# Optimization experiments

Hardware: AMD Instinct MI355X
Metric: run time of the kernel (lower is better)

The kernel has to match this reference:

```python
import jax, jax.numpy as jnp
import numpy as np

ALPHA = 1.702   # GLU sigmoid scale
LIMIT = 7.0     # clamp limit
K = 2           # experts per token


def setup_inputs() -> dict:
    key = jax.random.key(0)
    ks = jax.random.split(key, 4)
    B, S, H, E, I = 1, 1024, 1024, 8, 1024
    return {
        "hidden_states": jax.random.normal(ks[0], (B, S, H), jnp.float32),
        "router_weight": jax.random.normal(ks[1], (E, H), jnp.float32),
        "router_bias": jnp.zeros((E,), jnp.float32),
        "gate_up_proj": jax.random.normal(ks[2], (E, H, 2 * I), jnp.float32) * 0.02,
        "gate_up_bias": jnp.zeros((E, 2 * I), jnp.float32),
        "down_proj": jax.random.normal(ks[3], (E, I, H), jnp.float32) * 0.02,
        "down_bias": jnp.zeros((E, H), jnp.float32),
    }


def reference(hidden_states, router_weight, router_bias, gate_up_proj,
              gate_up_bias, down_proj, down_bias):
    B, S, H = hidden_states.shape
    E = router_weight.shape[0]
    I = down_proj.shape[1]
    T = B * S

    flat = hidden_states.reshape(T, H)

    # Router: softmax over experts, top-K selection (weights NOT renormalized).
    logits = flat @ router_weight.T + router_bias               # [T, E]
    scores = jax.nn.softmax(logits, axis=-1)
    topk_vals, topk_idx = jax.lax.top_k(scores, K)              # [T, K]

    # Dense per-token expert weight matrix (equivalent of dispatch metadata +
    # combine * topk_weights in the tt pipeline); top-k indices are unique.
    w = jnp.zeros((T, E), scores.dtype).at[
        jnp.arange(T)[:, None], topk_idx].set(topk_vals)        # [T, E]

    # Expert MLP with clamped GLU (gpt-oss style).
    gu = jnp.einsum('th,ehf->tef', flat, gate_up_proj) + gate_up_bias  # [T,E,2I]
    gate = jnp.minimum(gu[..., :I], LIMIT)
    up = jnp.clip(gu[..., I:], -LIMIT, LIMIT)
    glu = gate * jax.nn.sigmoid(gate * ALPHA)
    act = (up + 1.0) * glu                                       # [T, E, I]

    down = jnp.einsum('tei,eih->teh', act, down_proj) + down_bias  # [T, E, H]

    # Weighted combine over selected experts.
    out = jnp.einsum('teh,te->th', down, w)
    return out.reshape(B, S, H)
```

## Files before the change

kernel.cpp:

```cpp
#include <hip/hip_runtime.h>
#include <hip/hip_bf16.h>


typedef unsigned short u16;
typedef __attribute__((ext_vector_type(8))) __bf16 bf16x8;
typedef __attribute__((ext_vector_type(4))) float f32x4;

#define T_TOK 1024
#define H_DIM 1024
#define E_NUM 8
#define I_DIM 1024
#define ALPHA 1.702f
#define LIMIT 7.0f
#define LSTR 72

__device__ __forceinline__ u16 f2bf(float f) {
    unsigned u = __builtin_bit_cast(unsigned, f);
    u = (u + 0x7FFFu + ((u >> 16) & 1u)) >> 16;
    return (u16)u;
}

__device__ __forceinline__ unsigned pk2(float lo, float hi) {
#if defined(__has_builtin) && __has_builtin(__builtin_amdgcn_cvt_pk_bf16_f32)
    typedef __attribute__((ext_vector_type(2))) __bf16 bf16x2_t;
    bf16x2_t v = __builtin_amdgcn_cvt_pk_bf16_f32(lo, hi);
    return __builtin_bit_cast(unsigned, v);
#else
    return (unsigned)f2bf(lo) | ((unsigned)f2bf(hi) << 16);
#endif
}

__device__ __forceinline__ f32x4 mfma16(bf16x8 a, bf16x8 b, f32x4 c) {
    return __builtin_amdgcn_mfma_f32_16x16x32_bf16(a, b, c, 0, 0, 0);
}

__device__ __forceinline__ void expert_range(const int* counts, int e,
                                             int& cnt, int& abase) {
    int a = 0, c = 0;
#pragma unroll
    for (int i = 0; i < E_NUM; ++i) {
        int v = counts[i];
        if (i < e) a += v;
        if (i == e) c = v;
    }
    cnt = c; abase = a;
}

__global__ void k_zero(int* counts) {
    if (threadIdx.x < E_NUM) counts[threadIdx.x] = 0;
}

__global__ __launch_bounds__(256) void k_router(
    const float* __restrict__ x, const float* __restrict__ rw,
    const float* __restrict__ rb, const float* __restrict__ db,
    int* __restrict__ counts, int* __restrict__ tok_list,
    float* __restrict__ w_list, u16* __restrict__ xb,
    float* __restrict__ out)
{
    const int t = blockIdx.x;
    const int tid = threadIdx.x;
    const float4 xv = *(const float4*)(x + (size_t)t * H_DIM + tid * 4);

    *(uint2*)(xb + (size_t)t * H_DIM + tid * 4) =
        make_uint2(pk2(xv.x, xv.y), pk2(xv.z, xv.w));

    float p[E_NUM];
#pragma unroll
    for (int e = 0; e < E_NUM; ++e) {
        const float4 wv = *(const float4*)(rw + e * H_DIM + tid * 4);
        p[e] = xv.x * wv.x + xv.y * wv.y + xv.z * wv.z + xv.w * wv.w;
    }
#pragma unroll
    for (int off = 32; off; off >>= 1) {
#pragma unroll
        for (int e = 0; e < E_NUM; ++e) p[e] += __shfl_down(p[e], off, 64);
    }
    __shared__ float red[4][E_NUM];
    __shared__ int se[2];
    __shared__ float sw[2];
    const int lane = tid & 63, wvid = tid >> 6;
    if (lane == 0) {
#pragma unroll
        for (int e = 0; e < E_NUM; ++e) red[wvid][e] = p[e];
    }
    __syncthreads();
    if (tid == 0) {
        float lg[E_NUM];
#pragma unroll
        for (int e = 0; e < E_NUM; ++e)
            lg[e] = red[0][e] + red[1][e] + red[2][e] + red[3][e] + rb[e];
        float m1 = -1e30f, m2 = -1e30f; int i1 = 0, i2 = 0;
#pragma unroll
        for (int e = 0; e < E_NUM; ++e) {
            float l = lg[e];
            if (l > m1) { m2 = m1; i2 = i1; m1 = l; i1 = e; }
            else if (l > m2) { m2 = l; i2 = e; }
        }
        float s = 0.f;
#pragma unroll
        for (int e = 0; e < E_NUM; ++e) s += __expf(lg[e] - m1);
        const float w0 = 1.0f / s;
        const float w1 = __expf(m2 - m1) / s;
        int slot0 = atomicAdd(&counts[i1], 1);
        tok_list[i1 * T_TOK + slot0] = t;
        w_list[i1 * T_TOK + slot0] = w0;
        int slot1 = atomicAdd(&counts[i2], 1);
        tok_list[i2 * T_TOK + slot1] = t;
        w_list[i2 * T_TOK + slot1] = w1;
        se[0] = i1; se[1] = i2; sw[0] = w0; sw[1] = w1;
    }
    __syncthreads();
    const int e0 = se[0], e1 = se[1];
    const float w0 = sw[0], w1 = sw[1];
    const int c = tid * 4;
    float4 d0 = *(const float4*)(db + e0 * H_DIM + c);
    float4 d1 = *(const float4*)(db + e1 * H_DIM + c);
    float4 o;
    o.x = w0 * d0.x + w1 * d1.x;
    o.y = w0 * d0.y + w1 * d1.y;
    o.z = w0 * d0.z + w1 * d1.z;
    o.w = w0 * d0.w + w1 * d1.w;
    *(float4*)(out + (size_t)t * H_DIM + c) = o;
}

__global__ __launch_bounds__(256) void k_gateup(
    const float* __restrict__ gup, const float* __restrict__ gub,
    const int* __restrict__ counts, const int* __restrict__ tok_list,
    const u16* __restrict__ xb, u16* __restrict__ act)
{
    const int e = blockIdx.z;
    int cnt, abase;
    expert_range(counts, e, cnt, abase);
    const int m0 = blockIdx.y * 64;
    if (m0 >= cnt) return;
    const int n0 = blockIdx.x * 32;
    const int tid = threadIdx.x;

    __shared__ __align__(16) u16 As[64 * LSTR];
    __shared__ __align__(16) u16 Bs[64 * LSTR];
    unsigned* Bs32 = (unsigned*)Bs;

    const int arow_i = tid >> 2, akq = (tid & 3) * 16;
    const int aslot = m0 + arow_i;
    const int atok = (aslot < cnt) ? tok_list[e * T_TOK + aslot] : 0;
    const u16* asrc = xb + (size_t)atok * H_DIM + akq;
    u16* adst = &As[arow_i * LSTR + akq];

    const int kp = tid >> 3, q = tid & 7;
    const float* bgate = gup + ((size_t)e << 21) + n0 + q * 4;

    const int lane = tid & 63, wv = tid >> 6;
    const int fm = lane & 15, kg = lane >> 4;

    f32x4 accg[2], accu[2];
#pragma unroll
    for (int nt = 0; nt < 2; ++nt) {
        accg[nt] = (f32x4){0.f, 0.f, 0.f, 0.f};
        accu[nt] = (f32x4){0.f, 0.f, 0.f, 0.f};
    }

#define GU_LOAD(A0, A1, G0, G1, U0, U1, KB)                                    \
    {                                                                          \
        const u16* ap_ = asrc + (KB);                                          \
        A0 = *(const uint4*)(ap_);                                             \
        A1 = *(const uint4*)(ap_ + 8);                                         \
        const float* gp_ = bgate + (size_t)((KB) + 2 * kp) * 2048;             \
        G0 = *(const float4*)(gp_);                                            \
        G1 = *(const float4*)(gp_ + 2048);                                     \
        U0 = *(const float4*)(gp_ + 1024);                                     \
        U1 = *(const float4*)(gp_ + 3072);                                     \
    }
#define GU_STORE(A0, A1, G0, G1, U0, U1)                                       \
    {                                                                          \
        *(uint4*)adst       = A0;                                              \
        *(uint4*)(adst + 8) = A1;                                              \
        const float* g0_ = (const float*)&G0; const float* g1_ = (const float*)&G1; \
        const float* u0_ = (const float*)&U0; const float* u1_ = (const float*)&U1; \
        _Pragma("unroll")                                                      \
        for (int j = 0; j < 4; ++j) {                                          \
            Bs32[(q * 4 + j) * 36 + kp]        = pk2(g0_[j], g1_[j]);          \
            Bs32[(32 + q * 4 + j) * 36 + kp]   = pk2(u0_[j], u1_[j]);          \
        }                                                                      \
    }
#define GU_MFMA()                                                              \
    {                                                                          \
        _Pragma("unroll")                                                      \
        for (int sub = 0; sub < 2; ++sub) {                                    \
            bf16x8 af = *(const bf16x8*)&As[(wv * 16 + fm) * LSTR + sub * 32 + kg * 8]; \
            _Pragma("unroll")                                                  \
            for (int nt = 0; nt < 2; ++nt) {                                   \
                bf16x8 bg = *(const bf16x8*)&Bs[(nt * 16 + fm) * LSTR + sub * 32 + kg * 8]; \
                bf16x8 bu = *(const bf16x8*)&Bs[(32 + nt * 16 + fm) * LSTR + sub * 32 + kg * 8]; \
                accg[nt] = mfma16(af, bg, accg[nt]);                           \
                accu[nt] = mfma16(af, bu, accu[nt]);                           \
            }                                                                  \
        }                                                                      \
    }

    uint4 a0s0, a1s0, a0s1, a1s1;
    float4 g0s0, g1s0, u0s0, u1s0, g0s1, g1s1, u0s1, u1s1;
    GU_LOAD(a0s0, a1s0, g0s0, g1s0, u0s0, u1s0, 0);
    GU_LOAD(a0s1, a1s1, g0s1, g1s1, u0s1, u1s1, 64);

    for (int kb = 0; kb < H_DIM; kb += 128) {
        __syncthreads();
        GU_STORE(a0s0, a1s0, g0s0, g1s0, u0s0, u1s0);
        if (kb + 128 < H_DIM) GU_LOAD(a0s0, a1s0, g0s0, g1s0, u0s0, u1s0, kb + 128);
        __syncthreads();
        GU_MFMA();

        __syncthreads();
        GU_STORE(a0s1, a1s1, g0s1, g1s1, u0s1, u1s1);
        if (kb + 192 < H_DIM) GU_LOAD(a0s1, a1s1, g0s1, g1s1, u0s1, u1s1, kb + 192);
        __syncthreads();
        GU_MFMA();
    }
#undef GU_LOAD
#undef GU_STORE
#undef GU_MFMA

#pragma unroll
    for (int r = 0; r < 4; ++r) {
        int rowb = wv * 16 + kg * 4 + r;
        int slot = m0 + rowb;
        if (slot >= cnt) continue;
        size_t arow_o = (size_t)(abase + slot) * I_DIM;
#pragma unroll
        for (int nt = 0; nt < 2; ++nt) {
            int cn = n0 + nt * 16 + fm;
            float g = accg[nt][r] + gub[e * 2048 + cn];
            float u = accu[nt][r] + gub[e * 2048 + 1024 + cn];
            g = fminf(g, LIMIT);
            u = fminf(fmaxf(u, -LIMIT), LIMIT);
            float glu = g / (1.f + __expf(-ALPHA * g));
            act[arow_o + cn] = f2bf((u + 1.f) * glu);
        }
    }
}

__global__ __launch_bounds__(256) void k_down(
    const float* __restrict__ dp,
    const int* __restrict__ counts, const int* __restrict__ tok_list,
    const float* __restrict__ w_list,
    const u16* __restrict__ act, float* __restrict__ out)
{
    const int e = blockIdx.z & 7, ks = blockIdx.z >> 3;
    int cnt, abase;
    expert_range(counts, e, cnt, abase);
    const int m0 = blockIdx.y * 64;
    if (m0 >= cnt) return;
    const int n0 = blockIdx.x * 64;
    const int tid = threadIdx.x;

    __shared__ __align__(16) u16 As[64 * LSTR];
    __shared__ __align__(16) u16 Bs[64 * LSTR];
    unsigned* Bs32 = (unsigned*)Bs;

    const int arow_i = tid >> 2, akq = (tid & 3) * 16;
    const u16* asrc = act + (size_t)(abase + m0 + arow_i) * I_DIM + ks * 512 + akq;
    u16* adst = &As[arow_i * LSTR + akq];

    const int kp = tid >> 3, q = tid & 7;
    const float* bsrc = dp + ((size_t)e << 20) + (size_t)(ks * 512) * 1024 + n0 + q * 4;

    const int lane = tid & 63, wv = tid >> 6;
    const int fm = lane & 15, kg = lane >> 4;

    f32x4 acc[4];
#pragma unroll
    for (int nt = 0; nt < 4; ++nt) acc[nt] = (f32x4){0.f, 0.f, 0.f, 0.f};

#define DN_LOAD(A0, A1, B00, B01, B10, B11, KB)                                \
    {                                                                          \
        const u16* ap_ = asrc + (KB);                                          \
        A0 = *(const uint4*)(ap_);                                             \
        A1 = *(const uint4*)(ap_ + 8);                                         \
        const float* bp_ = bsrc + (size_t)((KB) + 2 * kp) * 1024;              \
        B00 = *(const float4*)(bp_);                                           \
        B01 = *(const float4*)(bp_ + 1024);                                    \
        B10 = *(const float4*)(bp_ + 32);                                      \
        B11 = *(const float4*)(bp_ + 1056);                                    \
    }
#define DN_STORE(A0, A1, B00, B01, B10, B11)                                   \
    {                                                                          \
        *(uint4*)adst       = A0;                                              \
        *(uint4*)(adst + 8) = A1;                                              \
        const float* b00_ = (const float*)&B00; const float* b01_ = (const float*)&B01; \
        const float* b10_ = (const float*)&B10; const float* b11_ = (const float*)&B11; \
        _Pragma("unroll")                                                      \
        for (int j = 0; j < 4; ++j) {                                          \
            Bs32[(q * 4 + j) * 36 + kp]      = pk2(b00_[j], b01_[j]);          \
            Bs32[(32 + q * 4 + j) * 36 + kp] = pk2(b10_[j], b11_[j]);          \
        }                                                                      \
    }
#define DN_MFMA()                                                              \
    {                                                                          \
        _Pragma("unroll")                                                      \
        for (int sub = 0; sub < 2; ++sub) {                                    \
            bf16x8 af = *(const bf16x8*)&As[(wv * 16 + fm) * LSTR + sub * 32 + kg * 8]; \
            _Pragma("unroll")                                                  \
            for (int nt = 0; nt < 4; ++nt) {                                   \
                bf16x8 b = *(const bf16x8*)&Bs[(nt * 16 + fm) * LSTR + sub * 32 + kg * 8]; \
                acc[nt] = mfma16(af, b, acc[nt]);                              \
            }                                                                  \
        }                                                                      \
    }

    uint4 a0s0, a1s0, a0s1, a1s1;
    float4 b00s0, b01s0, b10s0, b11s0, b00s1, b01s1, b10s1, b11s1;
    DN_LOAD(a0s0, a1s0, b00s0, b01s0, b10s0, b11s0, 0);
    DN_LOAD(a0s1, a1s1, b00s1, b01s1, b10s1, b11s1, 64);

    for (int kb = 0; kb < 512; kb += 128) {
        __syncthreads();
        DN_STORE(a0s0, a1s0, b00s0, b01s0, b10s0, b11s0);
        if (kb + 128 < 512) DN_LOAD(a0s0, a1s0, b00s0, b01s0, b10s0, b11s0, kb + 128);
        __syncthreads();
        DN_MFMA();

        __syncthreads();
        DN_STORE(a0s1, a1s1, b00s1, b01s1, b10s1, b11s1);
        if (kb + 192 < 512) DN_LOAD(a0s1, a1s1, b00s1, b01s1, b10s1, b11s1, kb + 192);
        __syncthreads();
        DN_MFMA();
    }
#undef DN_LOAD
#undef DN_STORE
#undef DN_MFMA

#pragma unroll
    for (int r = 0; r < 4; ++r) {
        int rowb = wv * 16 + kg * 4 + r;
        int slot = m0 + rowb;
        if (slot >= cnt) continue;
        float wgt = w_list[e * T_TOK + slot];
        int tok = tok_list[e * T_TOK + slot];
        float* orow = out + (size_t)tok * H_DIM + n0;
#pragma unroll
        for (int nt = 0; nt < 4; ++nt)
            atomicAdd(orow + nt * 16 + fm, acc[nt][r] * wgt);
    }
}

extern "C" void kernel_launch(void* const* d_in, const int* in_sizes, int n_in,
                              void* d_out, int out_size, void* d_ws, size_t ws_size,
                              hipStream_t stream) {
    const float* x   = (const float*)d_in[0];
    const float* rw  = (const float*)d_in[1];
    const float* rb  = (const float*)d_in[2];
    const float* gup = (const float*)d_in[3];
    const float* gub = (const float*)d_in[4];
    const float* dp  = (const float*)d_in[5];
    const float* db  = (const float*)d_in[6];
    float* out = (float*)d_out;

    char* ws = (char*)d_ws;
    int*   counts   = (int*)(ws);
    int*   tok_list = (int*)(ws + 64);
    float* w_list   = (float*)(ws + 64 + 32768);
    u16*   xb       = (u16*)(ws + 65600);
    u16*   act      = (u16*)(ws + 65600 + 2097152);

    k_zero<<<1, 64, 0, stream>>>(counts);
    k_router<<<T_TOK, 256, 0, stream>>>(x, rw, rb, db, counts, tok_list, w_list,
                                        xb, out);
    k_gateup<<<dim3(32, 16, 8), 256, 0, stream>>>(gup, gub, counts, tok_list,
                                                  xb, act);
    k_down<<<dim3(16, 16, 16), 256, 0, stream>>>(dp, counts, tok_list, w_list,
                                                 act, out);
}
```

Baseline: 212.0 us.

## Double-buffer LDS tiles and replace atomic combine with separate reduction kernel

The gate-up and down GEMM main loops now use two LDS buffers, so each step needs only one barrier instead of two and the next tile's store overlaps the current MFMA work. The down kernel writes weighted partial results per K-split into a scratch buffer instead of doing float atomicAdd into the output. A new combine kernel sums the two expert contributions and the two K-split partials per token and adds the bias. The zeroing kernel is replaced by a memset. This adds an extra launch and extra scratch-buffer traffic in exchange for removing atomic contention and halving barriers.

```diff
diff --git a/kernel.cpp b/kernel.cpp
--- a/kernel.cpp
+++ b/kernel.cpp
@@ -13,6 +13,8 @@
 #define ALPHA 1.702f
 #define LIMIT 7.0f
 #define LSTR 72
+#define AROWS 2112
+#define DPART (AROWS * 1024)
 
 __device__ __forceinline__ u16 f2bf(float f) {
     unsigned u = __builtin_bit_cast(unsigned, f);
@@ -46,16 +48,12 @@
     cnt = c; abase = a;
 }
 
-__global__ void k_zero(int* counts) {
-    if (threadIdx.x < E_NUM) counts[threadIdx.x] = 0;
-}
-
 __global__ __launch_bounds__(256) void k_router(
     const float* __restrict__ x, const float* __restrict__ rw,
-    const float* __restrict__ rb, const float* __restrict__ db,
-    int* __restrict__ counts, int* __restrict__ tok_list,
-    float* __restrict__ w_list, u16* __restrict__ xb,
-    float* __restrict__ out)
+    const float* __restrict__ rb,
+    int* __restrict__ counts, int* __restrict__ tk_e, int* __restrict__ tk_slot,
+    float* __restrict__ tk_w, int* __restrict__ tok_list,
+    float* __restrict__ w_list, u16* __restrict__ xb)
 {
     const int t = blockIdx.x;
     const int tid = threadIdx.x;
@@ -76,8 +74,6 @@
         for (int e = 0; e < E_NUM; ++e) p[e] += __shfl_down(p[e], off, 64);
     }
     __shared__ float red[4][E_NUM];
-    __shared__ int se[2];
-    __shared__ float sw[2];
     const int lane = tid & 63, wvid = tid >> 6;
     if (lane == 0) {
 #pragma unroll
@@ -101,26 +97,19 @@
         for (int e = 0; e < E_NUM; ++e) s += __expf(lg[e] - m1);
         const float w0 = 1.0f / s;
         const float w1 = __expf(m2 - m1) / s;
-        int slot0 = atomicAdd(&counts[i1], 1);
-        tok_list[i1 * T_TOK + slot0] = t;
-        w_list[i1 * T_TOK + slot0] = w0;
-        int slot1 = atomicAdd(&counts[i2], 1);
-        tok_list[i2 * T_TOK + slot1] = t;
-        w_list[i2 * T_TOK + slot1] = w1;
-        se[0] = i1; se[1] = i2; sw[0] = w0; sw[1] = w1;
-    }
-    __syncthreads();
-    const int e0 = se[0], e1 = se[1];
-    const float w0 = sw[0], w1 = sw[1];
-    const int c = tid * 4;
-    float4 d0 = *(const float4*)(db + e0 * H_DIM + c);
-    float4 d1 = *(const float4*)(db + e1 * H_DIM + c);
-    float4 o;
-    o.x = w0 * d0.x + w1 * d1.x;
-    o.y = w0 * d0.y + w1 * d1.y;
-    o.z = w0 * d0.z + w1 * d1.z;
-    o.w = w0 * d0.w + w1 * d1.w;
-    *(float4*)(out + (size_t)t * H_DIM + c) = o;
+        int ee[2] = { i1, i2 };
+        float ww[2] = { w0, w1 };
+#pragma unroll
+        for (int k = 0; k < 2; ++k) {
+            int e = ee[k];
+            int slot = atomicAdd(&counts[e], 1);
+            tok_list[e * T_TOK + slot] = t;
+            w_list[e * T_TOK + slot] = ww[k];
+            tk_e[t * 2 + k] = e;
+            tk_slot[t * 2 + k] = slot;
+            tk_w[t * 2 + k] = ww[k];
+        }
+    }
 }
 
 __global__ __launch_bounds__(256) void k_gateup(
@@ -136,15 +125,14 @@
     const int n0 = blockIdx.x * 32;
     const int tid = threadIdx.x;
 
-    __shared__ __align__(16) u16 As[64 * LSTR];
-    __shared__ __align__(16) u16 Bs[64 * LSTR];
-    unsigned* Bs32 = (unsigned*)Bs;
-
+    __shared__ __align__(16) u16 As[2][64 * LSTR];
+    __shared__ __align__(16) u16 Bs[2][64 * LSTR];
+    
     const int arow_i = tid >> 2, akq = (tid & 3) * 16;
     const int aslot = m0 + arow_i;
     const int atok = (aslot < cnt) ? tok_list[e * T_TOK + aslot] : 0;
     const u16* asrc = xb + (size_t)atok * H_DIM + akq;
-    u16* adst = &As[arow_i * LSTR + akq];
+    const int aoff = arow_i * LSTR + akq;
 
     const int kp = tid >> 3, q = tid & 7;
     const float* bgate = gup + ((size_t)e << 21) + n0 + q * 4;
@@ -159,61 +147,65 @@
         accu[nt] = (f32x4){0.f, 0.f, 0.f, 0.f};
     }
 
-#define GU_LOAD(A0, A1, G0, G1, U0, U1, KB)                                    \
-    {                                                                          \
-        const u16* ap_ = asrc + (KB);                                          \
+#define GU_LOAD(A0, A1, G0, G1, U0, U1, CH)                                    \
+    {                                                                          \
+        const u16* ap_ = asrc + (CH) * 64;                                     \
         A0 = *(const uint4*)(ap_);                                             \
         A1 = *(const uint4*)(ap_ + 8);                                         \
-        const float* gp_ = bgate + (size_t)((KB) + 2 * kp) * 2048;             \
+        const float* gp_ = bgate + (size_t)((CH) * 64 + 2 * kp) * 2048;        \
         G0 = *(const float4*)(gp_);                                            \
         G1 = *(const float4*)(gp_ + 2048);                                     \
         U0 = *(const float4*)(gp_ + 1024);                                     \
         U1 = *(const float4*)(gp_ + 3072);                                     \
     }
-#define GU_STORE(A0, A1, G0, G1, U0, U1)                                       \
-    {                                                                          \
-        *(uint4*)adst       = A0;                                              \
-        *(uint4*)(adst + 8) = A1;                                              \
+#define GU_STORE(BUF, A0, A1, G0, G1, U0, U1)                                  \
+    {                                                                          \
+        *(uint4*)&As[BUF][aoff]     = A0;                                      \
+        *(uint4*)&As[BUF][aoff + 8] = A1;                                      \
+        unsigned* b32_ = (unsigned*)&Bs[BUF][0];                               \
         const float* g0_ = (const float*)&G0; const float* g1_ = (const float*)&G1; \
         const float* u0_ = (const float*)&U0; const float* u1_ = (const float*)&U1; \
         _Pragma("unroll")                                                      \
         for (int j = 0; j < 4; ++j) {                                          \
-            Bs32[(q * 4 + j) * 36 + kp]        = pk2(g0_[j], g1_[j]);          \
-            Bs32[(32 + q * 4 + j) * 36 + kp]   = pk2(u0_[j], u1_[j]);          \
+            b32_[(q * 4 + j) * 36 + kp]      = pk2(g0_[j], g1_[j]);            \
+            b32_[(32 + q * 4 + j) * 36 + kp] = pk2(u0_[j], u1_[j]);            \
         }                                                                      \
     }
-#define GU_MFMA()                                                              \
+#define GU_MFMA(BUF)                                                           \
     {                                                                          \
         _Pragma("unroll")                                                      \
         for (int sub = 0; sub < 2; ++sub) {                                    \
-            bf16x8 af = *(const bf16x8*)&As[(wv * 16 + fm) * LSTR + sub * 32 + kg * 8]; \
+            bf16x8 af = *(const bf16x8*)&As[BUF][(wv * 16 + fm) * LSTR + sub * 32 + kg * 8]; \
             _Pragma("unroll")                                                  \
             for (int nt = 0; nt < 2; ++nt) {                                   \
-                bf16x8 bg = *(const bf16x8*)&Bs[(nt * 16 + fm) * LSTR + sub * 32 + kg * 8]; \
-                bf16x8 bu = *(const bf16x8*)&Bs[(32 + nt * 16 + fm) * LSTR + sub * 32 + kg * 8]; \
+                bf16x8 bg = *(const bf16x8*)&Bs[BUF][(nt * 16 + fm) * LSTR + sub * 32 + kg * 8]; \
+                bf16x8 bu = *(const bf16x8*)&Bs[BUF][(32 + nt * 16 + fm) * LSTR + sub * 32 + kg * 8]; \
                 accg[nt] = mfma16(af, bg, accg[nt]);                           \
                 accu[nt] = mfma16(af, bu, accu[nt]);                           \
             }                                                                  \
         }                                                                      \
     }
 
-    uint4 a0s0, a1s0, a0s1, a1s1;
-    float4 g0s0, g1s0, u0s0, u1s0, g0s1, g1s1, u0s1, u1s1;
-    GU_LOAD(a0s0, a1s0, g0s0, g1s0, u0s0, u1s0, 0);
-    GU_LOAD(a0s1, a1s1, g0s1, g1s1, u0s1, u1s1, 64);
-
-    for (int kb = 0; kb < H_DIM; kb += 128) {
+    uint4 a0r0, a1r0, a0r1, a1r1;
+    float4 g0r0, g1r0, u0r0, u1r0, g0r1, g1r1, u0r1, u1r1;
+    GU_LOAD(a0r0, a1r0, g0r0, g1r0, u0r0, u1r0, 0);
+    GU_LOAD(a0r1, a1r1, g0r1, g1r1, u0r1, u1r1, 1);
+    GU_STORE(0, a0r0, a1r0, g0r0, g1r0, u0r0, u1r0);
+    GU_LOAD(a0r0, a1r0, g0r0, g1r0, u0r0, u1r0, 2);
+
+#pragma unroll 4
+    for (int i = 0; i < 16; ++i) {
         __syncthreads();
-        GU_STORE(a0s0, a1s0, g0s0, g1s0, u0s0, u1s0);
-        if (kb + 128 < H_DIM) GU_LOAD(a0s0, a1s0, g0s0, g1s0, u0s0, u1s0, kb + 128);
-        __syncthreads();
-        GU_MFMA();
-
-        __syncthreads();
-        GU_STORE(a0s1, a1s1, g0s1, g1s1, u0s1, u1s1);
-        if (kb + 192 < H_DIM) GU_LOAD(a0s1, a1s1, g0s1, g1s1, u0s1, u1s1, kb + 192);
-        __syncthreads();
-        GU_MFMA();
+        const int b = i & 1;
+        if (i < 15) {
+            if (b == 0) { GU_STORE(1, a0r1, a1r1, g0r1, g1r1, u0r1, u1r1); }
+            else        { GU_STORE(0, a0r0, a1r0, g0r0, g1r0, u0r0, u1r0); }
+        }
+        if (i < 13) {
+            if (b == 0) { GU_LOAD(a0r1, a1r1, g0r1, g1r1, u0r1, u1r1, i + 3); }
+            else        { GU_LOAD(a0r0, a1r0, g0r0, g1r0, u0r0, u1r0, i + 3); }
+        }
+        GU_MFMA(b);
     }
 #undef GU_LOAD
 #undef GU_STORE
@@ -240,9 +232,8 @@
 
 __global__ __launch_bounds__(256) void k_down(
     const float* __restrict__ dp,
-    const int* __restrict__ counts, const int* __restrict__ tok_list,
-    const float* __restrict__ w_list,
-    const u16* __restrict__ act, float* __restrict__ out)
+    const int* __restrict__ counts, const float* __restrict__ w_list,
+    const u16* __restrict__ act, float* __restrict__ dout)
 {
     const int e = blockIdx.z & 7, ks = blockIdx.z >> 3;
     int cnt, abase;
@@ -252,13 +243,12 @@
     const int n0 = blockIdx.x * 64;
     const int tid = threadIdx.x;
 
-    __shared__ __align__(16) u16 As[64 * LSTR];
-    __shared__ __align__(16) u16 Bs[64 * LSTR];
-    unsigned* Bs32 = (unsigned*)Bs;
+    __shared__ __align__(16) u16 As[2][64 * LSTR];
+    __shared__ __align__(16) u16 Bs[2][64 * LSTR];
 
     const int arow_i = tid >> 2, akq = (tid & 3) * 16;
     const u16* asrc = act + (size_t)(abase + m0 + arow_i) * I_DIM + ks * 512 + akq;
-    u16* adst = &As[arow_i * LSTR + akq];
+    const int aoff = arow_i * LSTR + akq;
 
     const int kp = tid >> 3, q = tid & 7;
     const float* bsrc = dp + ((size_t)e << 20) + (size_t)(ks * 512) * 1024 + n0 + q * 4;
@@ -270,59 +260,63 @@
 #pragma unroll
     for (int nt = 0; nt < 4; ++nt) acc[nt] = (f32x4){0.f, 0.f, 0.f, 0.f};
 
-#define DN_LOAD(A0, A1, B00, B01, B10, B11, KB)                                \
-    {                                                                          \
-        const u16* ap_ = asrc + (KB);                                          \
+#define DN_LOAD(A0, A1, B00, B01, B10, B11, CH)                                \
+    {                                                                          \
+        const u16* ap_ = asrc + (CH) * 64;                                     \
         A0 = *(const uint4*)(ap_);                                             \
         A1 = *(const uint4*)(ap_ + 8);                                         \
-        const float* bp_ = bsrc + (size_t)((KB) + 2 * kp) * 1024;              \
+        const float* bp_ = bsrc + (size_t)((CH) * 64 + 2 * kp) * 1024;         \
         B00 = *(const float4*)(bp_);                                           \
         B01 = *(const float4*)(bp_ + 1024);                                    \
         B10 = *(const float4*)(bp_ + 32);                                      \
         B11 = *(const float4*)(bp_ + 1056);                                    \
     }
-#define DN_STORE(A0, A1, B00, B01, B10, B11)                                   \
-    {                                                                          \
-        *(uint4*)adst       = A0;                                              \
-        *(uint4*)(adst + 8) = A1;                                              \
+#define DN_STORE(BUF, A0, A1, B00, B01, B10, B11)                              \
+    {                                                                          \
+        *(uint4*)&As[BUF][aoff]     = A0;                                      \
+        *(uint4*)&As[BUF][aoff + 8] = A1;                                      \
+        unsigned* b32_ = (unsigned*)&Bs[BUF][0];                               \
         const float* b00_ = (const float*)&B00; const float* b01_ = (const float*)&B01; \
         const float* b10_ = (const float*)&B10; const float* b11_ = (const float*)&B11; \
         _Pragma("unroll")                                                      \
         for (int j = 0; j < 4; ++j) {                                          \
-            Bs32[(q * 4 + j) * 36 + kp]      = pk2(b00_[j], b01_[j]);          \
-            Bs32[(32 + q * 4 + j) * 36 + kp] = pk2(b10_[j], b11_[j]);          \
+            b32_[(q * 4 + j) * 36 + kp]      = pk2(b00_[j], b01_[j]);          \
+            b32_[(32 + q * 4 + j) * 36 + kp] = pk2(b10_[j], b11_[j]);          \
         }                                                                      \
     }
-#define DN_MFMA()                                                              \
+#define DN_MFMA(BUF)                                                           \
     {                                                                          \
         _Pragma("unroll")                                                      \
         for (int sub = 0; sub < 2; ++sub) {                                    \
-            bf16x8 af = *(const bf16x8*)&As[(wv * 16 + fm) * LSTR + sub * 32 + kg * 8]; \
+            bf16x8 af = *(const bf16x8*)&As[BUF][(wv * 16 + fm) * LSTR + sub * 32 + kg * 8]; \
             _Pragma("unroll")                                                  \
             for (int nt = 0; nt < 4; ++nt) {                                   \
-                bf16x8 b = *(const bf16x8*)&Bs[(nt * 16 + fm) * LSTR + sub * 32 + kg * 8]; \
-                acc[nt] = mfma16(af, b, acc[nt]);                              \
+                bf16x8 bb = *(const bf16x8*)&Bs[BUF][(nt * 16 + fm) * LSTR + sub * 32 + kg * 8]; \
+                acc[nt] = mfma16(af, bb, acc[nt]);                             \
             }                                                                  \
         }                                                                      \
     }
 
-    uint4 a0s0, a1s0, a0s1, a1s1;
-    float4 b00s0, b01s0, b10s0, b11s0, b00s1, b01s1, b10s1, b11s1;
-    DN_LOAD(a0s0, a1s0, b00s0, b01s0, b10s0, b11s0, 0);
-    DN_LOAD(a0s1, a1s1, b00s1, b01s1, b10s1, b11s1, 64);
-
-    for (int kb = 0; kb < 512; kb += 128) {
+    uint4 a0r0, a1r0, a0r1, a1r1;
+    float4 b00r0, b01r0, b10r0, b11r0, b00r1, b01r1, b10r1, b11r1;
+    DN_LOAD(a0r0, a1r0, b00r0, b01r0, b10r0, b11r0, 0);
+    DN_LOAD(a0r1, a1r1, b00r1, b01r1, b10r1, b11r1, 1);
+    DN_STORE(0, a0r0, a1r0, b00r0, b01r0, b10r0, b11r0);
+    DN_LOAD(a0r0, a1r0, b00r0, b01r0, b10r0, b11r0, 2);
+
+#pragma unroll 4
+    for (int i = 0; i < 8; ++i) {
         __syncthreads();
-        DN_STORE(a0s0, a1s0, b00s0, b01s0, b10s0, b11s0);
-        if (kb + 128 < 512) DN_LOAD(a0s0, a1s0, b00s0, b01s0, b10s0, b11s0, kb + 128);
-        __syncthreads();
-        DN_MFMA();
-
-        __syncthreads();
-        DN_STORE(a0s1, a1s1, b00s1, b01s1, b10s1, b11s1);
-        if (kb + 192 < 512) DN_LOAD(a0s1, a1s1, b00s1, b01s1, b10s1, b11s1, kb + 192);
-        __syncthreads();
-        DN_MFMA();
+        const int b = i & 1;
+        if (i < 7) {
+            if (b == 0) { DN_STORE(1, a0r1, a1r1, b00r1, b01r1, b10r1, b11r1); }
+            else        { DN_STORE(0, a0r0, a1r0, b00r0, b01r0, b10r0, b11r0); }
+        }
+        if (i < 5) {
+            if (b == 0) { DN_LOAD(a0r1, a1r1, b00r1, b01r1, b10r1, b11r1, i + 3); }
+            else        { DN_LOAD(a0r0, a1r0, b00r0, b01r0, b10r0, b11r0, i + 3); }
+        }
+        DN_MFMA(b);
     }
 #undef DN_LOAD
 #undef DN_STORE
@@ -334,12 +328,40 @@
         int slot = m0 + rowb;
         if (slot >= cnt) continue;
         float wgt = w_list[e * T_TOK + slot];
-        int tok = tok_list[e * T_TOK + slot];
-        float* orow = out + (size_t)tok * H_DIM + n0;
+        size_t drow = (size_t)ks * DPART + (size_t)(abase + slot) * H_DIM;
 #pragma unroll
         for (int nt = 0; nt < 4; ++nt)
-            atomicAdd(orow + nt * 16 + fm, acc[nt][r] * wgt);
-    }
+            dout[drow + n0 + nt * 16 + fm] = acc[nt][r] * wgt;
+    }
+}
+
+__global__ __launch_bounds__(256) void k_combine(
+    const float* __restrict__ dout, const float* __restrict__ db,
+    const int* __restrict__ counts,
+    const int* __restrict__ tk_e, const int* __restrict__ tk_slot,
+    const float* __restrict__ tk_w, float* __restrict__ out)
+{
+    const int t = blockIdx.x, tid = threadIdx.x;
+    const int e0 = tk_e[t * 2], e1 = tk_e[t * 2 + 1];
+    int c0, a0base, c1, a1base;
+    expert_range(counts, e0, c0, a0base);
+    expert_range(counts, e1, c1, a1base);
+    const size_t p0 = (size_t)(a0base + tk_slot[t * 2]) * H_DIM;
+    const size_t p1 = (size_t)(a1base + tk_slot[t * 2 + 1]) * H_DIM;
+    const float w0 = tk_w[t * 2], w1 = tk_w[t * 2 + 1];
+    const int c = tid * 4;
+    float4 x0 = *(const float4*)(dout + p0 + c);
+    float4 x1 = *(const float4*)(dout + DPART + p0 + c);
+    float4 y0 = *(const float4*)(dout + p1 + c);
+    float4 y1 = *(const float4*)(dout + DPART + p1 + c);
+    float4 d0 = *(const float4*)(db + e0 * H_DIM + c);
+    float4 d1 = *(const float4*)(db + e1 * H_DIM + c);
+    float4 o;
+    o.x = x0.x + x1.x + y0.x + y1.x + w0 * d0.x + w1 * d1.x;
+    o.y = x0.y + x1.y + y0.y + y1.y + w0 * d0.y + w1 * d1.y;
+    o.z = x0.z + x1.z + y0.z + y1.z + w0 * d0.z + w1 * d1.z;
+    o.w = x0.w + x1.w + y0.w + y1.w + w0 * d0.w + w1 * d1.w;
+    *(float4*)(out + (size_t)t * H_DIM + c) = o;
 }
 
 extern "C" void kernel_launch(void* const* d_in, const int* in_sizes, int n_in,
@@ -356,16 +378,21 @@
 
     char* ws = (char*)d_ws;
     int*   counts   = (int*)(ws);
-    int*   tok_list = (int*)(ws + 64);
-    float* w_list   = (float*)(ws + 64 + 32768);
-    u16*   xb       = (u16*)(ws + 65600);
-    u16*   act      = (u16*)(ws + 65600 + 2097152);
-
-    k_zero<<<1, 64, 0, stream>>>(counts);
-    k_router<<<T_TOK, 256, 0, stream>>>(x, rw, rb, db, counts, tok_list, w_list,
-                                        xb, out);
+    int*   tk_e     = (int*)(ws + 64);
+    int*   tk_slot  = (int*)(ws + 8256);
+    float* tk_w     = (float*)(ws + 16448);
+    int*   tok_list = (int*)(ws + 24640);
+    float* w_list   = (float*)(ws + 57408);
+    u16*   xb       = (u16*)(ws + 90176);
+    u16*   act      = (u16*)(ws + 90176 + 2097152);
+    float* dout     = (float*)(ws + 90176 + 2097152 + 4325376);
+
+    hipMemsetAsync(counts, 0, 64, stream);
+    k_router<<<T_TOK, 256, 0, stream>>>(x, rw, rb, counts, tk_e, tk_slot, tk_w,
+                                        tok_list, w_list, xb);
     k_gateup<<<dim3(32, 16, 8), 256, 0, stream>>>(gup, gub, counts, tok_list,
                                                   xb, act);
-    k_down<<<dim3(16, 16, 16), 256, 0, stream>>>(dp, counts, tok_list, w_list,
-                                                 act, out);
-}
+    k_down<<<dim3(16, 16, 16), 256, 0, stream>>>(dp, counts, w_list, act, dout);
+    k_combine<<<T_TOK, 256, 0, stream>>>(dout, db, counts, tk_e, tk_slot, tk_w,
+                                         out);
+}
```

Measured after the change: 214.5 us. About the same (+1.2%).

## Pre-transpose weights to bf16 and enlarge GEMM tiles with double-buffered LDS

Applied to the files above, without the earlier changes.

Adds a prep kernel that converts the gate_up and down weights to bf16 and transposes them into a K-contiguous layout on every call. The GEMM kernels can then load B tiles with plain 16-byte vector loads, with no per-element packing when writing to shared memory. The M tile grows from 64 to 128 rows so each B tile is reused across more tokens. Shared memory becomes double-buffered with one barrier per step, and k_zero is replaced by hipMemsetAsync. The cost is an extra pass that reads the full fp32 weights and writes about 50 MB of bf16, plus larger register and LDS use per block.

```diff
diff --git a/kernel.cpp b/kernel.cpp
--- a/kernel.cpp
+++ b/kernel.cpp
@@ -13,6 +13,7 @@
 #define ALPHA 1.702f
 #define LIMIT 7.0f
 #define LSTR 72
+#define AROWS 2176
 
 __device__ __forceinline__ u16 f2bf(float f) {
     unsigned u = __builtin_bit_cast(unsigned, f);
@@ -44,10 +45,6 @@
         if (i == e) c = v;
     }
     cnt = c; abase = a;
-}
-
-__global__ void k_zero(int* counts) {
-    if (threadIdx.x < E_NUM) counts[threadIdx.x] = 0;
 }
 
 __global__ __launch_bounds__(256) void k_router(
@@ -123,123 +120,184 @@
     *(float4*)(out + (size_t)t * H_DIM + c) = o;
 }
 
+__global__ __launch_bounds__(256) void k_prep(
+    const float* __restrict__ gup, const float* __restrict__ dp,
+    u16* __restrict__ gup_t, u16* __restrict__ dp_t)
+{
+    __shared__ unsigned Lt[64 * 36];
+    const int bid = blockIdx.x;
+    const float* src; u16* dst; int C, ct, kt;
+    if (bid < 4096) {
+        int e = bid >> 9, t = bid & 511;
+        ct = t & 31; kt = t >> 5; C = 2048;
+        src = gup + ((size_t)e << 21);
+        dst = gup_t + ((size_t)e << 21);
+    } else {
+        int b2 = bid - 4096;
+        int e = b2 >> 8, t = b2 & 255;
+        ct = t & 15; kt = t >> 4; C = 1024;
+        src = dp + ((size_t)e << 20);
+        dst = dp_t + ((size_t)e << 20);
+    }
+    const int k0 = kt * 64, c0 = ct * 64;
+    const int tid = threadIdx.x;
+
+    const int kp = tid >> 3, q = tid & 7;
+    const float* s0 = src + (size_t)(k0 + 2 * kp) * C + c0 + q * 8;
+    float4 r0a = *(const float4*)(s0);
+    float4 r0b = *(const float4*)(s0 + 4);
+    float4 r1a = *(const float4*)(s0 + C);
+    float4 r1b = *(const float4*)(s0 + C + 4);
+    const float* e0 = (const float*)&r0a;
+    const float* e1 = (const float*)&r0b;
+    const float* f0 = (const float*)&r1a;
+    const float* f1 = (const float*)&r1b;
+#pragma unroll
+    for (int j = 0; j < 8; ++j) {
+        float lo = (j < 4) ? e0[j] : e1[j - 4];
+        float hi = (j < 4) ? f0[j] : f1[j - 4];
+        int cl = q * 8 + j;
+        int grp = (kp >> 2) ^ q;
+        Lt[cl * 36 + (grp << 2) + (kp & 3)] = pk2(lo, hi);
+    }
+    __syncthreads();
+
+    const int cl = tid >> 2, ko2 = tid & 3;
+#pragma unroll
+    for (int i = 0; i < 2; ++i) {
+        int koct = ko2 * 2 + i;
+        int grp = koct ^ (cl >> 3);
+        uint4 v = *(const uint4*)&Lt[cl * 36 + (grp << 2)];
+        *(uint4*)(dst + (size_t)(c0 + cl) * 1024 + k0 + koct * 8) = v;
+    }
+}
+
 __global__ __launch_bounds__(256) void k_gateup(
-    const float* __restrict__ gup, const float* __restrict__ gub,
+    const u16* __restrict__ gup_t, const float* __restrict__ gub,
     const int* __restrict__ counts, const int* __restrict__ tok_list,
     const u16* __restrict__ xb, u16* __restrict__ act)
 {
     const int e = blockIdx.z;
     int cnt, abase;
     expert_range(counts, e, cnt, abase);
-    const int m0 = blockIdx.y * 64;
+    const int m0 = blockIdx.y * 128;
     if (m0 >= cnt) return;
     const int n0 = blockIdx.x * 32;
     const int tid = threadIdx.x;
 
-    __shared__ __align__(16) u16 As[64 * LSTR];
-    __shared__ __align__(16) u16 Bs[64 * LSTR];
-    unsigned* Bs32 = (unsigned*)Bs;
-
-    const int arow_i = tid >> 2, akq = (tid & 3) * 16;
+    __shared__ __align__(16) u16 As[2][128 * LSTR];
+    __shared__ __align__(16) u16 Bs[2][64 * LSTR];
+
+    const int arow_i = tid >> 1, akh = (tid & 1) * 32;
     const int aslot = m0 + arow_i;
     const int atok = (aslot < cnt) ? tok_list[e * T_TOK + aslot] : 0;
-    const u16* asrc = xb + (size_t)atok * H_DIM + akq;
-    u16* adst = &As[arow_i * LSTR + akq];
-
-    const int kp = tid >> 3, q = tid & 7;
-    const float* bgate = gup + ((size_t)e << 21) + n0 + q * 4;
+    const u16* asrc = xb + (size_t)atok * H_DIM + akh;
+    const int aoff = arow_i * LSTR + akh;
+
+    const int cl = tid >> 3, koct = tid & 7;
+    const u16* bgs = gup_t + ((size_t)(e * 2048 + n0 + cl)) * 1024 + koct * 8;
+    const u16* bus = bgs + (size_t)1024 * 1024;
+    const int boffg = cl * LSTR + koct * 8;
+    const int boffu = (32 + cl) * LSTR + koct * 8;
 
     const int lane = tid & 63, wv = tid >> 6;
     const int fm = lane & 15, kg = lane >> 4;
 
-    f32x4 accg[2], accu[2];
-#pragma unroll
-    for (int nt = 0; nt < 2; ++nt) {
-        accg[nt] = (f32x4){0.f, 0.f, 0.f, 0.f};
-        accu[nt] = (f32x4){0.f, 0.f, 0.f, 0.f};
-    }
-
-#define GU_LOAD(A0, A1, G0, G1, U0, U1, KB)                                    \
-    {                                                                          \
-        const u16* ap_ = asrc + (KB);                                          \
+    f32x4 accg[2][2], accu[2][2];
+#pragma unroll
+    for (int mt = 0; mt < 2; ++mt)
+#pragma unroll
+        for (int nt = 0; nt < 2; ++nt) {
+            accg[mt][nt] = (f32x4){0.f, 0.f, 0.f, 0.f};
+            accu[mt][nt] = (f32x4){0.f, 0.f, 0.f, 0.f};
+        }
+
+#define GU_LOAD(A0, A1, A2, A3, G, U, CH)                                      \
+    {                                                                          \
+        const u16* ap_ = asrc + (CH) * 64;                                     \
         A0 = *(const uint4*)(ap_);                                             \
         A1 = *(const uint4*)(ap_ + 8);                                         \
-        const float* gp_ = bgate + (size_t)((KB) + 2 * kp) * 2048;             \
-        G0 = *(const float4*)(gp_);                                            \
-        G1 = *(const float4*)(gp_ + 2048);                                     \
-        U0 = *(const float4*)(gp_ + 1024);                                     \
-        U1 = *(const float4*)(gp_ + 3072);                                     \
-    }
-#define GU_STORE(A0, A1, G0, G1, U0, U1)                                       \
-    {                                                                          \
-        *(uint4*)adst       = A0;                                              \
-        *(uint4*)(adst + 8) = A1;                                              \
-        const float* g0_ = (const float*)&G0; const float* g1_ = (const float*)&G1; \
-        const float* u0_ = (const float*)&U0; const float* u1_ = (const float*)&U1; \
-        _Pragma("unroll")                                                      \
-        for (int j = 0; j < 4; ++j) {                                          \
-            Bs32[(q * 4 + j) * 36 + kp]        = pk2(g0_[j], g1_[j]);          \
-            Bs32[(32 + q * 4 + j) * 36 + kp]   = pk2(u0_[j], u1_[j]);          \
-        }                                                                      \
-    }
-#define GU_MFMA()                                                              \
+        A2 = *(const uint4*)(ap_ + 16);                                        \
+        A3 = *(const uint4*)(ap_ + 24);                                        \
+        G = *(const uint4*)(bgs + (CH) * 64);                                  \
+        U = *(const uint4*)(bus + (CH) * 64);                                  \
+    }
+#define GU_STORE(BUF, A0, A1, A2, A3, G, U)                                    \
+    {                                                                          \
+        *(uint4*)&As[BUF][aoff]      = A0;                                     \
+        *(uint4*)&As[BUF][aoff + 8]  = A1;                                     \
+        *(uint4*)&As[BUF][aoff + 16] = A2;                                     \
+        *(uint4*)&As[BUF][aoff + 24] = A3;                                     \
+        *(uint4*)&Bs[BUF][boffg] = G;                                          \
+        *(uint4*)&Bs[BUF][boffu] = U;                                          \
+    }
+#define GU_MFMA(BUF)                                                           \
     {                                                                          \
         _Pragma("unroll")                                                      \
         for (int sub = 0; sub < 2; ++sub) {                                    \
-            bf16x8 af = *(const bf16x8*)&As[(wv * 16 + fm) * LSTR + sub * 32 + kg * 8]; \
             _Pragma("unroll")                                                  \
-            for (int nt = 0; nt < 2; ++nt) {                                   \
-                bf16x8 bg = *(const bf16x8*)&Bs[(nt * 16 + fm) * LSTR + sub * 32 + kg * 8]; \
-                bf16x8 bu = *(const bf16x8*)&Bs[(32 + nt * 16 + fm) * LSTR + sub * 32 + kg * 8]; \
-                accg[nt] = mfma16(af, bg, accg[nt]);                           \
-                accu[nt] = mfma16(af, bu, accu[nt]);                           \
+            for (int mt = 0; mt < 2; ++mt) {                                   \
+                bf16x8 af = *(const bf16x8*)&As[BUF][(wv * 32 + mt * 16 + fm) * LSTR + sub * 32 + kg * 8]; \
+                _Pragma("unroll")                                              \
+                for (int nt = 0; nt < 2; ++nt) {                               \
+                    bf16x8 bg = *(const bf16x8*)&Bs[BUF][(nt * 16 + fm) * LSTR + sub * 32 + kg * 8]; \
+                    bf16x8 bu = *(const bf16x8*)&Bs[BUF][(32 + nt * 16 + fm) * LSTR + sub * 32 + kg * 8]; \
+                    accg[mt][nt] = mfma16(af, bg, accg[mt][nt]);               \
+                    accu[mt][nt] = mfma16(af, bu, accu[mt][nt]);               \
+                }                                                              \
             }                                                                  \
         }                                                                      \
     }
 
-    uint4 a0s0, a1s0, a0s1, a1s1;
-    float4 g0s0, g1s0, u0s0, u1s0, g0s1, g1s1, u0s1, u1s1;
-    GU_LOAD(a0s0, a1s0, g0s0, g1s0, u0s0, u1s0, 0);
-    GU_LOAD(a0s1, a1s1, g0s1, g1s1, u0s1, u1s1, 64);
-
-    for (int kb = 0; kb < H_DIM; kb += 128) {
+    uint4 A0r0, A1r0, A2r0, A3r0, Gr0, Ur0;
+    uint4 A0r1, A1r1, A2r1, A3r1, Gr1, Ur1;
+    GU_LOAD(A0r0, A1r0, A2r0, A3r0, Gr0, Ur0, 0);
+    GU_LOAD(A0r1, A1r1, A2r1, A3r1, Gr1, Ur1, 1);
+    GU_STORE(0, A0r0, A1r0, A2r0, A3r0, Gr0, Ur0);
+    GU_LOAD(A0r0, A1r0, A2r0, A3r0, Gr0, Ur0, 2);
+
+#pragma unroll 4
+    for (int i = 0; i < 16; ++i) {
         __syncthreads();
-        GU_STORE(a0s0, a1s0, g0s0, g1s0, u0s0, u1s0);
-        if (kb + 128 < H_DIM) GU_LOAD(a0s0, a1s0, g0s0, g1s0, u0s0, u1s0, kb + 128);
-        __syncthreads();
-        GU_MFMA();
-
-        __syncthreads();
-        GU_STORE(a0s1, a1s1, g0s1, g1s1, u0s1, u1s1);
-        if (kb + 192 < H_DIM) GU_LOAD(a0s1, a1s1, g0s1, g1s1, u0s1, u1s1, kb + 192);
-        __syncthreads();
-        GU_MFMA();
+        const int b = i & 1;
+        if (i < 15) {
+            if (b == 0) { GU_STORE(1, A0r1, A1r1, A2r1, A3r1, Gr1, Ur1); }
+            else        { GU_STORE(0, A0r0, A1r0, A2r0, A3r0, Gr0, Ur0); }
+        }
+        if (i < 13) {
+            if (b == 0) { GU_LOAD(A0r1, A1r1, A2r1, A3r1, Gr1, Ur1, i + 3); }
+            else        { GU_LOAD(A0r0, A1r0, A2r0, A3r0, Gr0, Ur0, i + 3); }
+        }
+        GU_MFMA(b);
     }
 #undef GU_LOAD
 #undef GU_STORE
 #undef GU_MFMA
 
 #pragma unroll
-    for (int r = 0; r < 4; ++r) {
-        int rowb = wv * 16 + kg * 4 + r;
-        int slot = m0 + rowb;
-        if (slot >= cnt) continue;
-        size_t arow_o = (size_t)(abase + slot) * I_DIM;
-#pragma unroll
-        for (int nt = 0; nt < 2; ++nt) {
-            int cn = n0 + nt * 16 + fm;
-            float g = accg[nt][r] + gub[e * 2048 + cn];
-            float u = accu[nt][r] + gub[e * 2048 + 1024 + cn];
-            g = fminf(g, LIMIT);
-            u = fminf(fmaxf(u, -LIMIT), LIMIT);
-            float glu = g / (1.f + __expf(-ALPHA * g));
-            act[arow_o + cn] = f2bf((u + 1.f) * glu);
+    for (int mt = 0; mt < 2; ++mt) {
+#pragma unroll
+        for (int r = 0; r < 4; ++r) {
+            int rowb = wv * 32 + mt * 16 + kg * 4 + r;
+            int slot = m0 + rowb;
+            if (slot >= cnt) continue;
+            size_t arow_o = (size_t)(abase + slot) * I_DIM;
+#pragma unroll
+            for (int nt = 0; nt < 2; ++nt) {
+                int cn = n0 + nt * 16 + fm;
+                float g = accg[mt][nt][r] + gub[e * 2048 + cn];
+                float u = accu[mt][nt][r] + gub[e * 2048 + 1024 + cn];
+                g = fminf(g, LIMIT);
+                u = fminf(fmaxf(u, -LIMIT), LIMIT);
+                float glu = g / (1.f + __expf(-ALPHA * g));
+                act[arow_o + cn] = f2bf((u + 1.f) * glu);
+            }
         }
     }
 }
 
 __global__ __launch_bounds__(256) void k_down(
-    const float* __restrict__ dp,
+    const u16* __restrict__ dp_t,
     const int* __restrict__ counts, const int* __restrict__ tok_list,
     const float* __restrict__ w_list,
     const u16* __restrict__ act, float* __restrict__ out)
@@ -247,98 +305,107 @@
     const int e = blockIdx.z & 7, ks = blockIdx.z >> 3;
     int cnt, abase;
     expert_range(counts, e, cnt, abase);
-    const int m0 = blockIdx.y * 64;
+    const int m0 = blockIdx.y * 128;
     if (m0 >= cnt) return;
     const int n0 = blockIdx.x * 64;
     const int tid = threadIdx.x;
 
-    __shared__ __align__(16) u16 As[64 * LSTR];
-    __shared__ __align__(16) u16 Bs[64 * LSTR];
-    unsigned* Bs32 = (unsigned*)Bs;
-
-    const int arow_i = tid >> 2, akq = (tid & 3) * 16;
-    const u16* asrc = act + (size_t)(abase + m0 + arow_i) * I_DIM + ks * 512 + akq;
-    u16* adst = &As[arow_i * LSTR + akq];
-
-    const int kp = tid >> 3, q = tid & 7;
-    const float* bsrc = dp + ((size_t)e << 20) + (size_t)(ks * 512) * 1024 + n0 + q * 4;
+    __shared__ __align__(16) u16 As[2][128 * LSTR];
+    __shared__ __align__(16) u16 Bs[2][64 * LSTR];
+
+    const int arow_i = tid >> 1, akh = (tid & 1) * 32;
+    const u16* asrc = act + (size_t)(abase + m0 + arow_i) * I_DIM + ks * 512 + akh;
+    const int aoff = arow_i * LSTR + akh;
+
+    const int cl = tid >> 3, koct = tid & 7;
+    const u16* bs0 = dp_t + ((size_t)(e * 1024 + n0 + cl)) * 1024 + ks * 512 + koct * 8;
+    const u16* bs1 = bs0 + (size_t)32 * 1024;
+    const int boff0 = cl * LSTR + koct * 8;
+    const int boff1 = (32 + cl) * LSTR + koct * 8;
 
     const int lane = tid & 63, wv = tid >> 6;
     const int fm = lane & 15, kg = lane >> 4;
 
-    f32x4 acc[4];
-#pragma unroll
-    for (int nt = 0; nt < 4; ++nt) acc[nt] = (f32x4){0.f, 0.f, 0.f, 0.f};
-
-#define DN_LOAD(A0, A1, B00, B01, B10, B11, KB)                                \
-    {                                                                          \
-        const u16* ap_ = asrc + (KB);                                          \
+    f32x4 acc[2][4];
+#pragma unroll
+    for (int mt = 0; mt < 2; ++mt)
+#pragma unroll
+        for (int nt = 0; nt < 4; ++nt) acc[mt][nt] = (f32x4){0.f, 0.f, 0.f, 0.f};
+
+#define DN_LOAD(A0, A1, A2, A3, B0, B1, CH)                                    \
+    {                                                                          \
+        const u16* ap_ = asrc + (CH) * 64;                                     \
         A0 = *(const uint4*)(ap_);                                             \
         A1 = *(const uint4*)(ap_ + 8);                                         \
-        const float* bp_ = bsrc + (size_t)((KB) + 2 * kp) * 1024;              \
-        B00 = *(const float4*)(bp_);                                           \
-        B01 = *(const float4*)(bp_ + 1024);                                    \
-        B10 = *(const float4*)(bp_ + 32);                                      \
-        B11 = *(const float4*)(bp_ + 1056);                                    \
-    }
-#define DN_STORE(A0, A1, B00, B01, B10, B11)                                   \
-    {                                                                          \
-        *(uint4*)adst       = A0;                                              \
-        *(uint4*)(adst + 8) = A1;                                              \
-        const float* b00_ = (const float*)&B00; const float* b01_ = (const float*)&B01; \
-        const float* b10_ = (const float*)&B10; const float* b11_ = (const float*)&B11; \
-        _Pragma("unroll")                                                      \
-        for (int j = 0; j < 4; ++j) {                                          \
-            Bs32[(q * 4 + j) * 36 + kp]      = pk2(b00_[j], b01_[j]);          \
-            Bs32[(32 + q * 4 + j) * 36 + kp] = pk2(b10_[j], b11_[j]);          \
-        }                                                                      \
-    }
-#define DN_MFMA()                                                              \
+        A2 = *(const uint4*)(ap_ + 16);                                        \
+        A3 = *(const uint4*)(ap_ + 24);                                        \
+        B0 = *(const uint4*)(bs0 + (CH) * 64);                                 \
+        B1 = *(const uint4*)(bs1 + (CH) * 64);                                 \
+    }
+#define DN_STORE(BUF, A0, A1, A2, A3, B0, B1)                                  \
+    {                                                                          \
+        *(uint4*)&As[BUF][aoff]      = A0;                                     \
+        *(uint4*)&As[BUF][aoff + 8]  = A1;                                     \
+        *(uint4*)&As[BUF][aoff + 16] = A2;                                     \
+        *(uint4*)&As[BUF][aoff + 24] = A3;                                     \
+        *(uint4*)&Bs[BUF][boff0] = B0;                                         \
+        *(uint4*)&Bs[BUF][boff1] = B1;                                         \
+    }
+#define DN_MFMA(BUF)                                                           \
     {                                                                          \
         _Pragma("unroll")                                                      \
         for (int sub = 0; sub < 2; ++sub) {                                    \
-            bf16x8 af = *(const bf16x8*)&As[(wv * 16 + fm) * LSTR + sub * 32 + kg * 8]; \
             _Pragma("unroll")                                                  \
-            for (int nt = 0; nt < 4; ++nt) {                                   \
-                bf16x8 b = *(const bf16x8*)&Bs[(nt * 16 + fm) * LSTR + sub * 32 + kg * 8]; \
-                acc[nt] = mfma16(af, b, acc[nt]);                              \
+            for (int mt = 0; mt < 2; ++mt) {                                   \
+                bf16x8 af = *(const bf16x8*)&As[BUF][(wv * 32 + mt * 16 + fm) * LSTR + sub * 32 + kg * 8]; \
+                _Pragma("unroll")                                              \
+                for (int nt = 0; nt < 4; ++nt) {                               \
+                    bf16x8 bb = *(const bf16x8*)&Bs[BUF][(nt * 16 + fm) * LSTR + sub * 32 + kg * 8]; \
+                    acc[mt][nt] = mfma16(af, bb, acc[mt][nt]);                 \
+                }                                                              \
             }                                                                  \
         }                                                                      \
     }
 
-    uint4 a0s0, a1s0, a0s1, a1s1;
-    float4 b00s0, b01s0, b10s0, b11s0, b00s1, b01s1, b10s1, b11s1;
-    DN_LOAD(a0s0, a1s0, b00s0, b01s0, b10s0, b11s0, 0);
-    DN_LOAD(a0s1, a1s1, b00s1, b01s1, b10s1, b11s1, 64);
-
-    for (int kb = 0; kb < 512; kb += 128) {
+    uint4 A0r0, A1r0, A2r0, A3r0, B0r0, B1r0;
+    uint4 A0r1, A1r1, A2r1, A3r1, B0r1, B1r1;
+    DN_LOAD(A0r0, A1r0, A2r0, A3r0, B0r0, B1r0, 0);
+    DN_LOAD(A0r1, A1r1, A2r1, A3r1, B0r1, B1r1, 1);
+    DN_STORE(0, A0r0, A1r0, A2r0, A3r0, B0r0, B1r0);
+    DN_LOAD(A0r0, A1r0, A2r0, A3r0, B0r0, B1r0, 2);
+
+#pragma unroll 4
+    for (int i = 0; i < 8; ++i) {
         __syncthreads();
-        DN_STORE(a0s0, a1s0, b00s0, b01s0, b10s0, b11s0);
-        if (kb + 128 < 512) DN_LOAD(a0s0, a1s0, b00s0, b01s0, b10s0, b11s0, kb + 128);
-        __syncthreads();
-        DN_MFMA();
-
-        __syncthreads();
-        DN_STORE(a0s1, a1s1, b00s1, b01s1, b10s1, b11s1);
-        if (kb + 192 < 512) DN_LOAD(a0s1, a1s1, b00s1, b01s1, b10s1, b11s1, kb + 192);
-        __syncthreads();
-        DN_MFMA();
+        const int b = i & 1;
+        if (i < 7) {
+            if (b == 0) { DN_STORE(1, A0r1, A1r1, A2r1, A3r1, B0r1, B1r1); }
+            else        { DN_STORE(0, A0r0, A1r0, A2r0, A3r0, B0r0, B1r0); }
+        }
+        if (i < 5) {
+            if (b == 0) { DN_LOAD(A0r1, A1r1, A2r1, A3r1, B0r1, B1r1, i + 3); }
+            else        { DN_LOAD(A0r0, A1r0, A2r0, A3r0, B0r0, B1r0, i + 3); }
+        }
+        DN_MFMA(b);
     }
 #undef DN_LOAD
 #undef DN_STORE
 #undef DN_MFMA
 
 #pragma unroll
-    for (int r = 0; r < 4; ++r) {
-        int rowb = wv * 16 + kg * 4 + r;
-        int slot = m0 + rowb;
-        if (slot >= cnt) continue;
-        float wgt = w_list[e * T_TOK + slot];
-        int tok = tok_list[e * T_TOK + slot];
-        float* orow = out + (size_t)tok * H_DIM + n0;
-#pragma unroll
-        for (int nt = 0; nt < 4; ++nt)
-            atomicAdd(orow + nt * 16 + fm, acc[nt][r] * wgt);
+    for (int mt = 0; mt < 2; ++mt) {
+#pragma unroll
+        for (int r = 0; r < 4; ++r) {
+            int rowb = wv * 32 + mt * 16 + kg * 4 + r;
+            int slot = m0 + rowb;
+            if (slot >= cnt) continue;
+            float wgt = w_list[e * T_TOK + slot];
+            int tok = tok_list[e * T_TOK + slot];
+            float* orow = out + (size_t)tok * H_DIM + n0;
+#pragma unroll
+            for (int nt = 0; nt < 4; ++nt)
+                atomicAdd(orow + nt * 16 + fm, acc[mt][nt][r] * wgt);
+        }
     }
 }
 
@@ -357,15 +424,18 @@
     char* ws = (char*)d_ws;
     int*   counts   = (int*)(ws);
     int*   tok_list = (int*)(ws + 64);
-    float* w_list   = (float*)(ws + 64 + 32768);
+    float* w_list   = (float*)(ws + 32832);
     u16*   xb       = (u16*)(ws + 65600);
-    u16*   act      = (u16*)(ws + 65600 + 2097152);
-
-    k_zero<<<1, 64, 0, stream>>>(counts);
+    u16*   gup_t    = (u16*)(ws + 2162752);
+    u16*   dp_t     = (u16*)(ws + 35717184);
+    u16*   act      = (u16*)(ws + 52494400);
+
+    hipMemsetAsync(counts, 0, 64, stream);
     k_router<<<T_TOK, 256, 0, stream>>>(x, rw, rb, db, counts, tok_list, w_list,
                                         xb, out);
-    k_gateup<<<dim3(32, 16, 8), 256, 0, stream>>>(gup, gub, counts, tok_list,
-                                                  xb, act);
-    k_down<<<dim3(16, 16, 16), 256, 0, stream>>>(dp, counts, tok_list, w_list,
-                                                 act, out);
-}
+    k_prep<<<6144, 256, 0, stream>>>(gup, dp, gup_t, dp_t);
+    k_gateup<<<dim3(32, 8, 8), 256, 0, stream>>>(gup_t, gub, counts, tok_list,
+                                                 xb, act);
+    k_down<<<dim3(16, 8, 16), 256, 0, stream>>>(dp_t, counts, tok_list, w_list,
+                                                act, out);
+}
```

Measured after the change: 234.6 us. 10.7% more time.
